# Optimization experiments

Measured on AMD Instinct MI355X. Metric: run time of the kernel, lower is better.

The kernel has to match this reference:

```python
import jax, jax.numpy as jnp
import numpy as np

B, S, H, C = 8, 4096, 768, 64  # batch, seq_len, hidden_dim, block size


def _xavier(k, shape):
    fan = shape[0] + shape[1]
    return jax.random.normal(k, shape, jnp.float32) * np.sqrt(2.0 / fan)


def setup_inputs() -> dict:
    key = jax.random.key(0)
    kx, kq, kk, kv, k1, k2 = jax.random.split(key, 6)
    return {
        "x": jax.random.normal(kx, (B, S, H), jnp.float32),
        "Wq": _xavier(kq, (H, H)),
        "Wk": _xavier(kk, (H, H)),
        "Wv": _xavier(kv, (H, H)),
        "W1": _xavier(k1, (H, 16)),
        "W2": _xavier(k2, (16, H)),
        "b": jnp.zeros((H,), jnp.float32),
    }


def reference(x, Wq, Wk, Wv, W1, W2, b):
    Bb, Ss, Hh = x.shape
    NB = Ss // C  # number of blocks (seq_len divisible by C, no remainder)
    Q = x @ Wq
    K = x @ Wk
    V = x @ Wv
    # gating alpha: identical every block iteration in the original, compute once
    alpha = jax.nn.sigmoid((x @ W1) @ W2 + b) ** (1.0 / 16.0)  # [B,S,H]
    a = alpha.mean(axis=1, keepdims=True)  # [B,1,H], broadcasts over rows of state
    # blocks to leading axis for scan: [NB, B, C, H]
    qs = Q.reshape(Bb, NB, C, Hh).transpose(1, 0, 2, 3)
    ks = K.reshape(Bb, NB, C, Hh).transpose(1, 0, 2, 3)
    vs = V.reshape(Bb, NB, C, Hh).transpose(1, 0, 2, 3)
    mask = jnp.tril(jnp.ones((C, C), x.dtype))
    scale = 1.0 / np.sqrt(Hh).astype(np.float32)

    def step(St, blk):
        qb, kb, vb = blk  # each [B,C,H]
        # state update first (original updates S before computing output)
        St = St * a + jnp.einsum("bch,bcd->bhd", kb, vb)  # [B,H,H]
        # intra-block: scores masked by MULTIPLICATION (as in original), then softmax
        scores = jnp.einsum("bch,bdh->bcd", qb, kb) * mask * scale
        w = jax.nn.softmax(scores, axis=-1)
        out = jnp.einsum("bch,bhd->bcd", qb, St) + jnp.einsum("bcd,bde->bce", w, vb)
        return St, out

    S0 = jnp.zeros((Bb, Hh, Hh), x.dtype)
    _, outs = jax.lax.scan(step, S0, (qs, ks, vs))  # outs: [NB,B,C,H]
    O = outs.transpose(1, 0, 2, 3).reshape(Bb, Ss, Hh)
    return O
```

## Files before the change

### kernel.cpp

```cpp
#include <hip/hip_runtime.h>

#define B_ 8
#define S_ 4096
#define H_ 768
#define C_ 64
#define NB_ 64
#define M_ (B_*S_)

#define NCH_ 8
#define LCH_ 8

typedef _Float16 f16x8 __attribute__((ext_vector_type(8)));
typedef _Float16 f16x4 __attribute__((ext_vector_type(4)));
typedef float    f32x4 __attribute__((ext_vector_type(4)));

__global__ __launch_bounds__(256) void k_transpose(const float* __restrict__ src,
                                                   _Float16* __restrict__ dst) {
  __shared__ float tile[32][33];
  const int t = threadIdx.x;
  const int tx = t & 31, ty = t >> 5;
  const int n0 = blockIdx.x * 32, k0 = blockIdx.y * 32;
#pragma unroll
  for (int i = 0; i < 4; ++i)
    tile[ty + i*8][tx] = src[(k0 + ty + i*8) * H_ + n0 + tx];
  __syncthreads();
#pragma unroll
  for (int i = 0; i < 4; ++i)
    dst[(n0 + ty + i*8) * H_ + k0 + tx] = (_Float16)tile[tx][ty + i*8];
}

__global__ __launch_bounds__(256) void k_gemm_qkv(
    const float* __restrict__ x,
    const _Float16* __restrict__ WqT, const _Float16* __restrict__ WkT,
    const _Float16* __restrict__ WvT,
    _Float16* __restrict__ Qb,
    _Float16* __restrict__ KT, _Float16* __restrict__ VT) {
  __shared__ _Float16 xs[64][40];
  __shared__ _Float16 ws[3][128][40];
  const int t = threadIdx.x;
  const int m0 = blockIdx.x * 64, n0 = blockIdx.y * 128;
  const int lane = t & 63, wv = t >> 6;
  const int lm = lane & 15, qd = lane >> 4;
  const int sm = t >> 2, sk = (t & 3) * 8;
  const int wn = t >> 1, wk = (t & 1) * 16;

  f32x4 acc[3][4][2];
#pragma unroll
  for (int a = 0; a < 3; ++a)
#pragma unroll
    for (int i = 0; i < 4; ++i)
#pragma unroll
      for (int n = 0; n < 2; ++n)
        acc[a][i][n] = (f32x4){0.f, 0.f, 0.f, 0.f};

  for (int kk = 0; kk < 24; ++kk) {
    const int k0 = kk * 32;
    __syncthreads();
    {
      const f32x4* xp = (const f32x4*)&x[(size_t)(m0 + sm) * H_ + k0 + sk];
      f32x4 f0 = xp[0], f1 = xp[1];
      f16x8 xv;
#pragma unroll
      for (int j = 0; j < 4; ++j) { xv[j] = (_Float16)f0[j]; xv[4 + j] = (_Float16)f1[j]; }
      *(f16x8*)&xs[sm][sk] = xv;
    }
    {
      const f16x8* wp = (const f16x8*)&WqT[(n0 + wn) * H_ + k0 + wk];
      *(f16x8*)&ws[0][wn][wk] = wp[0]; *(f16x8*)&ws[0][wn][wk + 8] = wp[1];
      wp = (const f16x8*)&WkT[(n0 + wn) * H_ + k0 + wk];
      *(f16x8*)&ws[1][wn][wk] = wp[0]; *(f16x8*)&ws[1][wn][wk + 8] = wp[1];
      wp = (const f16x8*)&WvT[(n0 + wn) * H_ + k0 + wk];
      *(f16x8*)&ws[2][wn][wk] = wp[0]; *(f16x8*)&ws[2][wn][wk + 8] = wp[1];
    }
    __syncthreads();
    f16x8 af[4];
#pragma unroll
    for (int i = 0; i < 4; ++i) af[i] = *(f16x8*)&xs[i*16 + lm][qd*8];
#pragma unroll
    for (int a = 0; a < 3; ++a)
#pragma unroll
      for (int n = 0; n < 2; ++n) {
        f16x8 bfr = *(f16x8*)&ws[a][wv*32 + n*16 + lm][qd*8];
#pragma unroll
        for (int i = 0; i < 4; ++i)
          acc[a][i][n] = __builtin_amdgcn_mfma_f32_16x16x32_f16(af[i], bfr, acc[a][i][n], 0, 0, 0);
      }
  }
#pragma unroll
  for (int i = 0; i < 4; ++i)
#pragma unroll
    for (int n = 0; n < 2; ++n) {
      const int ng = n0 + wv*32 + n*16 + lm;
      const int mg0 = m0 + i*16 + qd*4;
      const int bb = mg0 >> 12, ss = mg0 & (S_ - 1);
#pragma unroll
      for (int r = 0; r < 4; ++r)
        Qb[(size_t)(mg0 + r) * H_ + ng] = (_Float16)acc[0][i][n][r];
      f16x4 kp, vp;
#pragma unroll
      for (int r = 0; r < 4; ++r) {
        kp[r] = (_Float16)acc[1][i][n][r];
        vp[r] = (_Float16)acc[2][i][n][r];
      }
      *(f16x4*)&KT[((size_t)bb * H_ + ng) * S_ + ss] = kp;
      *(f16x4*)&VT[((size_t)bb * H_ + ng) * S_ + ss] = vp;
    }
}

__global__ __launch_bounds__(256) void k_tgemm(const float* __restrict__ x,
                                               const float* __restrict__ W1,
                                               float* __restrict__ tbuf) {
  __shared__ float w1s[768 * 16];
  __shared__ float xs[64 * 129];
  const int t = threadIdx.x;
  const int m0 = blockIdx.x * 64;
  for (int i = t; i < 768 * 16 / 4; i += 256)
    ((f32x4*)w1s)[i] = ((const f32x4*)W1)[i];
  const int row = t & 63, cg = t >> 6;
  f32x4 acc = (f32x4){0.f, 0.f, 0.f, 0.f};
  for (int kc = 0; kc < 768; kc += 128) {
    __syncthreads();
    for (int i = 0; i < 32; ++i) {
      const int idx = t + 256 * i;
      const int r = idx >> 7, c = idx & 127;
      xs[r * 129 + c] = x[(size_t)(m0 + r) * H_ + kc + c];
    }
    __syncthreads();
#pragma unroll 8
    for (int kl = 0; kl < 128; ++kl) {
      const float a = xs[row * 129 + kl];
      const f32x4 w = *(const f32x4*)&w1s[(kc + kl) * 16 + cg * 4];
#pragma unroll
      for (int j = 0; j < 4; ++j) acc[j] += a * w[j];
    }
  }
  *(f32x4*)&tbuf[(size_t)(m0 + row) * 16 + cg * 4] = acc;
}

__global__ __launch_bounds__(256) void k_areduce(const float* __restrict__ tbuf,
                                                 const float* __restrict__ W2,
                                                 const float* __restrict__ bias,
                                                 float* __restrict__ abuf) {
  __shared__ float ts[128 * 17];
  __shared__ float rbuf[8 * 32];
  const int t = threadIdx.x;
  const int b = blockIdx.y, hc = blockIdx.x;
  const int hl = t & 31, sg = t >> 5;
  const int h = hc * 32 + hl;
  float w2r[16];
#pragma unroll
  for (int j = 0; j < 16; ++j) w2r[j] = W2[j * H_ + h];
  const float bb = bias[h];
  float asum = 0.f;
  const float* tb = &tbuf[(size_t)(b * S_) * 16];
  for (int sc = 0; sc < S_; sc += 128) {
    __syncthreads();
    for (int i = 0; i < 8; ++i) {
      const int idx = t + 256 * i;
      const int sl = idx >> 4, j = idx & 15;
      ts[sl * 17 + j] = tb[(size_t)(sc + sl) * 16 + j];
    }
    __syncthreads();
    for (int i = 0; i < 16; ++i) {
      const int sl = sg + i * 8;
      float z = bb;
      const float* tr = &ts[sl * 17];
#pragma unroll
      for (int j = 0; j < 16; ++j) z += tr[j] * w2r[j];
      const float sgm = 1.f / (1.f + __expf(-z));
      asum += sqrtf(sqrtf(sqrtf(sqrtf(sgm))));
    }
  }
  rbuf[sg * 32 + hl] = asum;
  __syncthreads();
  if (t < 32) {
    float s = 0.f;
#pragma unroll
    for (int g = 0; g < 8; ++g) s += rbuf[g * 32 + t];
    abuf[b * H_ + hc * 32 + t] = s * (1.f / (float)S_);
  }
}

__global__ __launch_bounds__(256) void k_scores_y(
    const _Float16* __restrict__ Qb, const _Float16* __restrict__ KT,
    const _Float16* __restrict__ VT, float* __restrict__ O) {
  __shared__ float qs[64 * 68];
  __shared__ float ks[64 * 68];
  __shared__ float wb[64 * 68];
  __shared__ float vsb[64 * 68];
  const int t = threadIdx.x;
  const int nb = blockIdx.x, b = blockIdx.y;
  const size_t base = ((size_t)b * S_ + nb * 64) * H_;
  const int tc = t >> 4, td = t & 15;
  const int srow = t >> 2, sseg = (t & 3) * 16;

  float scr[4][4];
#pragma unroll
  for (int i = 0; i < 4; ++i)
#pragma unroll
    for (int u = 0; u < 4; ++u) scr[i][u] = 0.f;

  for (int hc = 0; hc < 12; ++hc) {
    __syncthreads();
    {
      const f16x8* qp = (const f16x8*)&Qb[base + (size_t)srow * H_ + hc * 64 + sseg];
      f16x8 q0 = qp[0], q1 = qp[1];
#pragma unroll
      for (int j = 0; j < 8; ++j) {
        qs[(sseg + j) * 68 + srow] = (float)q0[j];
        qs[(sseg + 8 + j) * 68 + srow] = (float)q1[j];
      }
    }
    {
      const size_t krow = ((size_t)b * H_ + hc * 64 + srow) * S_ + nb * 64 + sseg;
      f16x8 k0 = *(const f16x8*)&KT[krow];
      f16x8 k1 = *(const f16x8*)&KT[krow + 8];
      f32x4 f;
#pragma unroll
      for (int j = 0; j < 4; ++j) f[j] = (float)k0[j];
      *(f32x4*)&ks[srow * 68 + sseg] = f;
#pragma unroll
      for (int j = 0; j < 4; ++j) f[j] = (float)k0[4 + j];
      *(f32x4*)&ks[srow * 68 + sseg + 4] = f;
#pragma unroll
      for (int j = 0; j < 4; ++j) f[j] = (float)k1[j];
      *(f32x4*)&ks[srow * 68 + sseg + 8] = f;
#pragma unroll
      for (int j = 0; j < 4; ++j) f[j] = (float)k1[4 + j];
      *(f32x4*)&ks[srow * 68 + sseg + 12] = f;
    }
    __syncthreads();
#pragma unroll 4
    for (int h = 0; h < 64; ++h) {
      const f32x4 qv = *(f32x4*)&qs[h * 68 + tc * 4];
      const f32x4 kv = *(f32x4*)&ks[h * 68 + td * 4];
#pragma unroll
      for (int i = 0; i < 4; ++i)
#pragma unroll
        for (int u = 0; u < 4; ++u) scr[i][u] += qv[i] * kv[u];
    }
  }
  const float scale = 0.036084391824351615f;
#pragma unroll
  for (int i = 0; i < 4; ++i)
#pragma unroll
    for (int u = 0; u < 4; ++u) {
      const int c = tc * 4 + i, d = td * 4 + u;
      wb[d * 68 + c] = (d <= c) ? scr[i][u] * scale : 0.f;
    }
  __syncthreads();
  {
    const int r = t >> 2, g = t & 3;
    float vals[16];
    float mx = -1e30f;
#pragma unroll
    for (int i = 0; i < 16; ++i) {
      vals[i] = wb[(g * 16 + i) * 68 + r];
      mx = fmaxf(mx, vals[i]);
    }
    mx = fmaxf(mx, __shfl_xor(mx, 1));
    mx = fmaxf(mx, __shfl_xor(mx, 2));
    float sm = 0.f;
#pragma unroll
    for (int i = 0; i < 16; ++i) { vals[i] = __expf(vals[i] - mx); sm += vals[i]; }
    sm += __shfl_xor(sm, 1);
    sm += __shfl_xor(sm, 2);
    const float inv = 1.f / sm;
#pragma unroll
    for (int i = 0; i < 16; ++i) wb[(g * 16 + i) * 68 + r] = vals[i] * inv;
  }
  for (int ec = 0; ec < 12; ++ec) {
    __syncthreads();
    {
      const size_t vrow = ((size_t)b * H_ + ec * 64 + srow) * S_ + nb * 64 + sseg;
      f16x8 v0 = *(const f16x8*)&VT[vrow];
      f16x8 v1 = *(const f16x8*)&VT[vrow + 8];
#pragma unroll
      for (int j = 0; j < 8; ++j) {
        vsb[(sseg + j) * 68 + srow] = (float)v0[j];
        vsb[(sseg + 8 + j) * 68 + srow] = (float)v1[j];
      }
    }
    __syncthreads();
    float y[4][4];
#pragma unroll
    for (int i = 0; i < 4; ++i)
#pragma unroll
      for (int u = 0; u < 4; ++u) y[i][u] = 0.f;
#pragma unroll 4
    for (int j = 0; j < 64; ++j) {
      const f32x4 wv = *(f32x4*)&wb[j * 68 + tc * 4];
      const f32x4 vv = *(f32x4*)&vsb[j * 68 + td * 4];
#pragma unroll
      for (int i = 0; i < 4; ++i)
#pragma unroll
        for (int u = 0; u < 4; ++u) y[i][u] += wv[i] * vv[u];
    }
#pragma unroll
    for (int i = 0; i < 4; ++i) {
      f32x4 yv = {y[i][0], y[i][1], y[i][2], y[i][3]};
      *(f32x4*)&O[base + (size_t)(tc * 4 + i) * H_ + ec * 64 + td * 4] = yv;
    }
  }
}

__global__ __launch_bounds__(256, 2) void k_scan_chunk(
    const _Float16* __restrict__ KT, const _Float16* __restrict__ VT,
    const float* __restrict__ abuf, _Float16* __restrict__ Tb) {
  const int t = threadIdx.x;
  const int b = blockIdx.z, ch = blockIdx.y, dt = blockIdx.x;
  const int d0 = dt * 32;
  const int w = t >> 6, lane = t & 63;
  const int lm = lane & 15, qd = lane >> 4;

  const float av0 = abuf[b * H_ + d0 + lm];
  const float av1 = abuf[b * H_ + d0 + 16 + lm];

  f32x4 acc[12][2];
#pragma unroll
  for (int mt = 0; mt < 12; ++mt) {
    acc[mt][0] = (f32x4){0.f, 0.f, 0.f, 0.f};
    acc[mt][1] = (f32x4){0.f, 0.f, 0.f, 0.f};
  }

  const size_t ktb = (size_t)b * H_ * S_;
  const size_t vrow0 = ktb + (size_t)(d0 + lm) * S_;
  const size_t vrow1 = ktb + (size_t)(d0 + 16 + lm) * S_;

  for (int blk = ch * LCH_; blk < ch * LCH_ + LCH_; ++blk) {
    const int s0 = blk * 64;
    f16x8 vf00 = *(const f16x8*)&VT[vrow0 + s0 + qd * 8];
    f16x8 vf01 = *(const f16x8*)&VT[vrow0 + s0 + 32 + qd * 8];
    f16x8 vf10 = *(const f16x8*)&VT[vrow1 + s0 + qd * 8];
    f16x8 vf11 = *(const f16x8*)&VT[vrow1 + s0 + 32 + qd * 8];
#pragma unroll
    for (int mt = 0; mt < 12; ++mt) {
      const size_t arow = ktb + (size_t)((w * 12 + mt) * 16 + lm) * S_ + s0 + qd * 8;
      f16x8 a0 = *(const f16x8*)&KT[arow];
      f16x8 a1 = *(const f16x8*)&KT[arow + 32];
      f32x4 c0 = acc[mt][0] * av0;
      f32x4 c1 = acc[mt][1] * av1;
      c0 = __builtin_amdgcn_mfma_f32_16x16x32_f16(a0, vf00, c0, 0, 0, 0);
      c0 = __builtin_amdgcn_mfma_f32_16x16x32_f16(a1, vf01, c0, 0, 0, 0);
      c1 = __builtin_amdgcn_mfma_f32_16x16x32_f16(a0, vf10, c1, 0, 0, 0);
      c1 = __builtin_amdgcn_mfma_f32_16x16x32_f16(a1, vf11, c1, 0, 0, 0);
      acc[mt][0] = c0;
      acc[mt][1] = c1;
    }
  }
  _Float16* tp = Tb + ((((size_t)b * NCH_ + ch) * 24 + dt) * 32) * 768;
#pragma unroll
  for (int mt = 0; mt < 12; ++mt) {
    const int h = (w * 12 + mt) * 16 + qd * 4;
    f16x4 p0, p1;
#pragma unroll
    for (int r = 0; r < 4; ++r) {
      p0[r] = (_Float16)acc[mt][0][r];
      p1[r] = (_Float16)acc[mt][1][r];
    }
    *(f16x4*)&tp[(size_t)lm * 768 + h] = p0;
    *(f16x4*)&tp[(size_t)(16 + lm) * 768 + h] = p1;
  }
}

__global__ __launch_bounds__(256) void k_combine(const float* __restrict__ abuf,
                                                 _Float16* __restrict__ Tb) {
  const int gid = blockIdx.x * 256 + threadIdx.x;
  const int hv = gid % 96;
  const int dl = (gid / 96) & 31;
  const int dt = (gid / (96 * 32)) % 24;
  const int b  = gid / (96 * 32 * 24);
  const float ad = abuf[b * H_ + dt * 32 + dl];
  const float a2 = ad * ad, a4 = a2 * a2;
  const float aL = a4 * a4;
  float carry[8];
#pragma unroll
  for (int j = 0; j < 8; ++j) carry[j] = 0.f;
  const size_t chstride = (size_t)24 * 32 * 768;
  _Float16* p = Tb + (size_t)b * NCH_ * chstride + ((size_t)dt * 32 + dl) * 768 + hv * 8;
  for (int ch = 0; ch < NCH_; ++ch, p += chstride) {
    const f16x8 tv = *(const f16x8*)p;
    f16x8 cv;
#pragma unroll
    for (int j = 0; j < 8; ++j) {
      cv[j] = (_Float16)carry[j];
      carry[j] = carry[j] * aL + (float)tv[j];
    }
    *(f16x8*)p = cv;
  }
}

#define STP 776
__global__ __launch_bounds__(256, 2) void k_scan_out(
    const _Float16* __restrict__ Qb, const _Float16* __restrict__ KT,
    const _Float16* __restrict__ VT, const float* __restrict__ abuf,
    const _Float16* __restrict__ Tb, float* __restrict__ O) {
  __shared__ _Float16 StL[32 * STP];
  const int t = threadIdx.x;
  const int b = blockIdx.z, ch = blockIdx.y, dt = blockIdx.x;
  const int d0 = dt * 32;
  const int w = t >> 6, lane = t & 63;
  const int lm = lane & 15, qd = lane >> 4;

  const float av0 = abuf[b * H_ + d0 + lm];
  const float av1 = abuf[b * H_ + d0 + 16 + lm];

  f32x4 acc[12][2];
  {
    const _Float16* tp = Tb + ((((size_t)b * NCH_ + ch) * 24 + dt) * 32) * 768;
#pragma unroll
    for (int mt = 0; mt < 12; ++mt) {
      const int h = (w * 12 + mt) * 16 + qd * 4;
      const f16x4 c0 = *(const f16x4*)&tp[(size_t)lm * 768 + h];
      const f16x4 c1 = *(const f16x4*)&tp[(size_t)(16 + lm) * 768 + h];
#pragma unroll
      for (int r = 0; r < 4; ++r) {
        acc[mt][0][r] = (float)c0[r];
        acc[mt][1][r] = (float)c1[r];
      }
    }
  }

  const size_t ktb = (size_t)b * H_ * S_;
  const size_t vrow0 = ktb + (size_t)(d0 + lm) * S_;
  const size_t vrow1 = ktb + (size_t)(d0 + 16 + lm) * S_;

  for (int blk = ch * LCH_; blk < ch * LCH_ + LCH_; ++blk) {
    const int s0 = blk * 64;
    f16x8 vf00 = *(const f16x8*)&VT[vrow0 + s0 + qd * 8];
    f16x8 vf01 = *(const f16x8*)&VT[vrow0 + s0 + 32 + qd * 8];
    f16x8 vf10 = *(const f16x8*)&VT[vrow1 + s0 + qd * 8];
    f16x8 vf11 = *(const f16x8*)&VT[vrow1 + s0 + 32 + qd * 8];
#pragma unroll
    for (int mt = 0; mt < 12; ++mt) {
      const size_t arow = ktb + (size_t)((w * 12 + mt) * 16 + lm) * S_ + s0 + qd * 8;
      f16x8 a0 = *(const f16x8*)&KT[arow];
      f16x8 a1 = *(const f16x8*)&KT[arow + 32];
      f32x4 c0 = acc[mt][0] * av0;
      f32x4 c1 = acc[mt][1] * av1;
      c0 = __builtin_amdgcn_mfma_f32_16x16x32_f16(a0, vf00, c0, 0, 0, 0);
      c0 = __builtin_amdgcn_mfma_f32_16x16x32_f16(a1, vf01, c0, 0, 0, 0);
      c1 = __builtin_amdgcn_mfma_f32_16x16x32_f16(a0, vf10, c1, 0, 0, 0);
      c1 = __builtin_amdgcn_mfma_f32_16x16x32_f16(a1, vf11, c1, 0, 0, 0);
      acc[mt][0] = c0;
      acc[mt][1] = c1;
    }
    __syncthreads();
#pragma unroll
    for (int mt = 0; mt < 12; ++mt) {
      const int h = (w * 12 + mt) * 16 + qd * 4;
      f16x4 p0, p1;
#pragma unroll
      for (int r = 0; r < 4; ++r) {
        p0[r] = (_Float16)acc[mt][0][r];
        p1[r] = (_Float16)acc[mt][1][r];
      }
      *(f16x4*)&StL[lm * STP + h] = p0;
      *(f16x4*)&StL[(16 + lm) * STP + h] = p1;
    }
    __syncthreads();
    f32x4 o0a = {0.f,0.f,0.f,0.f}, o0b = {0.f,0.f,0.f,0.f};
    f32x4 o1a = {0.f,0.f,0.f,0.f}, o1b = {0.f,0.f,0.f,0.f};
    const size_t qrow = ((size_t)b * S_ + s0 + w * 16 + lm) * H_ + qd * 8;
#pragma unroll 3
    for (int kt = 0; kt < 24; kt += 2) {
      f16x8 qa = *(const f16x8*)&Qb[qrow + kt * 32];
      f16x8 qb2 = *(const f16x8*)&Qb[qrow + kt * 32 + 32];
      f16x8 s00 = *(f16x8*)&StL[lm * STP + kt * 32 + qd * 8];
      f16x8 s01 = *(f16x8*)&StL[(16 + lm) * STP + kt * 32 + qd * 8];
      f16x8 s10 = *(f16x8*)&StL[lm * STP + kt * 32 + 32 + qd * 8];
      f16x8 s11 = *(f16x8*)&StL[(16 + lm) * STP + kt * 32 + 32 + qd * 8];
      o0a = __builtin_amdgcn_mfma_f32_16x16x32_f16(qa, s00, o0a, 0, 0, 0);
      o1a = __builtin_amdgcn_mfma_f32_16x16x32_f16(qa, s01, o1a, 0, 0, 0);
      o0b = __builtin_amdgcn_mfma_f32_16x16x32_f16(qb2, s10, o0b, 0, 0, 0);
      o1b = __builtin_amdgcn_mfma_f32_16x16x32_f16(qb2, s11, o1b, 0, 0, 0);
    }
    const f32x4 o0 = o0a + o0b;
    const f32x4 o1 = o1a + o1b;
    const size_t orow = ((size_t)b * S_ + s0 + w * 16 + qd * 4) * H_ + d0;
#pragma unroll
    for (int r = 0; r < 4; ++r) {
      O[orow + (size_t)r * H_ + lm] += o0[r];
      O[orow + (size_t)r * H_ + 16 + lm] += o1[r];
    }
  }
}

extern "C" void kernel_launch(void* const* d_in, const int* in_sizes, int n_in,
                              void* d_out, int out_size, void* d_ws, size_t ws_size,
                              hipStream_t stream) {
  (void)in_sizes; (void)n_in; (void)out_size; (void)ws_size;
  const float* x    = (const float*)d_in[0];
  const float* Wq   = (const float*)d_in[1];
  const float* Wk   = (const float*)d_in[2];
  const float* Wv   = (const float*)d_in[3];
  const float* W1   = (const float*)d_in[4];
  const float* W2   = (const float*)d_in[5];
  const float* bias = (const float*)d_in[6];
  float* O = (float*)d_out;

  char* ws = (char*)d_ws;
  _Float16* Qb  = (_Float16*)ws;
  _Float16* KT  = Qb + (size_t)M_ * H_;
  _Float16* VT  = KT + (size_t)M_ * H_;
  _Float16* WqT = VT + (size_t)M_ * H_;
  _Float16* WkT = WqT + H_ * H_;
  _Float16* WvT = WkT + H_ * H_;
  float* tbuf = (float*)(WvT + H_ * H_);
  float* abuf = tbuf + (size_t)M_ * 16;
  _Float16* Tb = (_Float16*)(abuf + B_ * H_);

  k_transpose<<<dim3(24, 24), 256, 0, stream>>>(Wq, WqT);
  k_transpose<<<dim3(24, 24), 256, 0, stream>>>(Wk, WkT);
  k_transpose<<<dim3(24, 24), 256, 0, stream>>>(Wv, WvT);
  k_gemm_qkv<<<dim3(512, 6), 256, 0, stream>>>(x, WqT, WkT, WvT, Qb, KT, VT);
  k_tgemm<<<dim3(512), 256, 0, stream>>>(x, W1, tbuf);
  k_areduce<<<dim3(24, 8), 256, 0, stream>>>(tbuf, W2, bias, abuf);
  k_scores_y<<<dim3(64, 8), 256, 0, stream>>>(Qb, KT, VT, O);
  k_scan_chunk<<<dim3(24, NCH_, 8), 256, 0, stream>>>(KT, VT, abuf, Tb);
  k_combine<<<dim3(2304), 256, 0, stream>>>(abuf, Tb);
  k_scan_out<<<dim3(24, NCH_, 8), 256, 0, stream>>>(Qb, KT, VT, abuf, Tb, O);
}
```

Baseline: 1.449 ms.

## Replace sequential chunk-state recurrence with decay-weighted GEMM using LDS-staged K tiles

```diff
diff --git a/kernel.cpp b/kernel.cpp
--- a/kernel.cpp
+++ b/kernel.cpp
@@ -304,63 +304,62 @@
   }
 }
 
-__global__ __launch_bounds__(256, 2) void k_scan_chunk(
+__global__ __launch_bounds__(256, 2) void k_chunk_gemm(
     const _Float16* __restrict__ KT, const _Float16* __restrict__ VT,
     const float* __restrict__ abuf, _Float16* __restrict__ Tb) {
-  const int t = threadIdx.x;
-  const int b = blockIdx.z, ch = blockIdx.y, dt = blockIdx.x;
-  const int d0 = dt * 32;
+  __shared__ _Float16 bs[128][40];
+  const int t = threadIdx.x;
+  const int b = blockIdx.y;
+  const int ch = blockIdx.x & 7, tile = blockIdx.x >> 3;
+  const int dt = tile / 6, ht = tile % 6;
   const int w = t >> 6, lane = t & 63;
   const int lm = lane & 15, qd = lane >> 4;
-
-  const float av0 = abuf[b * H_ + d0 + lm];
-  const float av1 = abuf[b * H_ + d0 + 16 + lm];
-
-  f32x4 acc[12][2];
-#pragma unroll
-  for (int mt = 0; mt < 12; ++mt) {
-    acc[mt][0] = (f32x4){0.f, 0.f, 0.f, 0.f};
-    acc[mt][1] = (f32x4){0.f, 0.f, 0.f, 0.f};
-  }
+  const int d0 = dt * 128 + w * 32;
+  const int h0 = ht * 128;
+  const int hrow = t >> 1, hseg = (t & 1) * 16;
+
+  float av[2], pw[2];
+  av[0] = abuf[b * H_ + d0 + lm];
+  av[1] = abuf[b * H_ + d0 + 16 + lm];
+  pw[0] = 1.f; pw[1] = 1.f;
+
+  f32x4 acc[2][8];
+#pragma unroll
+  for (int ds = 0; ds < 2; ++ds)
+#pragma unroll
+    for (int hh = 0; hh < 8; ++hh) acc[ds][hh] = (f32x4){0.f, 0.f, 0.f, 0.f};
 
   const size_t ktb = (size_t)b * H_ * S_;
-  const size_t vrow0 = ktb + (size_t)(d0 + lm) * S_;
-  const size_t vrow1 = ktb + (size_t)(d0 + 16 + lm) * S_;
-
-  for (int blk = ch * LCH_; blk < ch * LCH_ + LCH_; ++blk) {
-    const int s0 = blk * 64;
-    f16x8 vf00 = *(const f16x8*)&VT[vrow0 + s0 + qd * 8];
-    f16x8 vf01 = *(const f16x8*)&VT[vrow0 + s0 + 32 + qd * 8];
-    f16x8 vf10 = *(const f16x8*)&VT[vrow1 + s0 + qd * 8];
-    f16x8 vf11 = *(const f16x8*)&VT[vrow1 + s0 + 32 + qd * 8];
-#pragma unroll
-    for (int mt = 0; mt < 12; ++mt) {
-      const size_t arow = ktb + (size_t)((w * 12 + mt) * 16 + lm) * S_ + s0 + qd * 8;
-      f16x8 a0 = *(const f16x8*)&KT[arow];
-      f16x8 a1 = *(const f16x8*)&KT[arow + 32];
-      f32x4 c0 = acc[mt][0] * av0;
-      f32x4 c1 = acc[mt][1] * av1;
-      c0 = __builtin_amdgcn_mfma_f32_16x16x32_f16(a0, vf00, c0, 0, 0, 0);
-      c0 = __builtin_amdgcn_mfma_f32_16x16x32_f16(a1, vf01, c0, 0, 0, 0);
-      c1 = __builtin_amdgcn_mfma_f32_16x16x32_f16(a0, vf10, c1, 0, 0, 0);
-      c1 = __builtin_amdgcn_mfma_f32_16x16x32_f16(a1, vf11, c1, 0, 0, 0);
-      acc[mt][0] = c0;
-      acc[mt][1] = c1;
-    }
-  }
-  _Float16* tp = Tb + ((((size_t)b * NCH_ + ch) * 24 + dt) * 32) * 768;
-#pragma unroll
-  for (int mt = 0; mt < 12; ++mt) {
-    const int h = (w * 12 + mt) * 16 + qd * 4;
-    f16x4 p0, p1;
-#pragma unroll
-    for (int r = 0; r < 4; ++r) {
-      p0[r] = (_Float16)acc[mt][0][r];
-      p1[r] = (_Float16)acc[mt][1][r];
-    }
-    *(f16x4*)&tp[(size_t)lm * 768 + h] = p0;
-    *(f16x4*)&tp[(size_t)(16 + lm) * 768 + h] = p1;
-  }
+  for (int kk = 15; kk >= 0; --kk) {
+    const int sp = ch * 512 + kk * 32;
+    __syncthreads();
+    {
+      const f16x8* kp = (const f16x8*)&KT[ktb + (size_t)(h0 + hrow) * S_ + sp + hseg];
+      *(f16x8*)&bs[hrow][hseg] = kp[0];
+      *(f16x8*)&bs[hrow][hseg + 8] = kp[1];
+    }
+    __syncthreads();
+    f16x8 va0 = *(const f16x8*)&VT[ktb + (size_t)(d0 + lm) * S_ + sp + qd * 8];
+    f16x8 va1 = *(const f16x8*)&VT[ktb + (size_t)(d0 + 16 + lm) * S_ + sp + qd * 8];
+    va0 *= (_Float16)pw[0];
+    va1 *= (_Float16)pw[1];
+#pragma unroll
+    for (int hh = 0; hh < 8; ++hh) {
+      const f16x8 kf = *(const f16x8*)&bs[hh * 16 + lm][qd * 8];
+      acc[0][hh] = __builtin_amdgcn_mfma_f32_16x16x32_f16(va0, kf, acc[0][hh], 0, 0, 0);
+      acc[1][hh] = __builtin_amdgcn_mfma_f32_16x16x32_f16(va1, kf, acc[1][hh], 0, 0, 0);
+    }
+    if (!(kk & 1)) { pw[0] *= av[0]; pw[1] *= av[1]; }
+  }
+  _Float16* tp = Tb + (size_t)(b * NCH_ + ch) * 768 * 768;
+#pragma unroll
+  for (int ds = 0; ds < 2; ++ds)
+#pragma unroll
+    for (int hh = 0; hh < 8; ++hh)
+#pragma unroll
+      for (int r = 0; r < 4; ++r)
+        tp[(size_t)(d0 + ds * 16 + qd * 4 + r) * 768 + h0 + hh * 16 + lm] =
+            (_Float16)acc[ds][hh][r];
 }
 
 __global__ __launch_bounds__(256) void k_combine(const float* __restrict__ abuf,
@@ -513,11 +512,11 @@
   k_transpose<<<dim3(24, 24), 256, 0, stream>>>(Wq, WqT);
   k_transpose<<<dim3(24, 24), 256, 0, stream>>>(Wk, WkT);
   k_transpose<<<dim3(24, 24), 256, 0, stream>>>(Wv, WvT);
-  k_gemm_qkv<<<dim3(512, 6), 256, 0, stream>>>(x, WqT, WkT, WvT, Qb, KT, VT);
   k_tgemm<<<dim3(512), 256, 0, stream>>>(x, W1, tbuf);
   k_areduce<<<dim3(24, 8), 256, 0, stream>>>(tbuf, W2, bias, abuf);
+  k_gemm_qkv<<<dim3(512, 6), 256, 0, stream>>>(x, WqT, WkT, WvT, Qb, KT, VT);
   k_scores_y<<<dim3(64, 8), 256, 0, stream>>>(Qb, KT, VT, O);
-  k_scan_chunk<<<dim3(24, NCH_, 8), 256, 0, stream>>>(KT, VT, abuf, Tb);
+  k_chunk_gemm<<<dim3(288, 8), 256, 0, stream>>>(KT, VT, abuf, Tb);
   k_combine<<<dim3(2304), 256, 0, stream>>>(abuf, Tb);
   k_scan_out<<<dim3(24, NCH_, 8), 256, 0, stream>>>(Qb, KT, VT, abuf, Tb, O);
 }
```

Result: faster. 1.300 ms (-10.3%).
